# Kernel optimization log

Hardware: AMD Instinct MI355X
Metric: run time of the kernel (lower is better)

Reference implementation:

```python
import jax, jax.numpy as jnp
import numpy as np

I16_MIN, I16_MAX = -32768, 32767
NUM_SEG = 8


def setup_inputs() -> dict:
    key = jax.random.key(0)
    k1, k2, k3, k4, k5, k6 = jax.random.split(key, 6)
    # Float activation; quantized to qint16 inside the op via input_scale.
    x = jax.random.normal(k1, (16, 1024, 2048), dtype=jnp.float32)
    input_scale = jnp.full((1,), 1.0 / 8192.0, dtype=jnp.float32)  # randn*8192 spans most of int16
    out_scale = jnp.full((1,), 1e-3, dtype=jnp.float32)
    # Per-segment fixed-point linear coefficients (as produced by _convert_linear_kb / toqint):
    # 16-bit k, wide b pre-shifted by left_shift, result right-shifted by right_shift.
    alpha = jax.random.randint(k2, (NUM_SEG,), -4096, 4096, dtype=jnp.int32)        # int16 k
    beta = jax.random.randint(k3, (NUM_SEG,), -(1 << 20), 1 << 20, dtype=jnp.int32)  # int b
    left_shift = jax.random.randint(k4, (NUM_SEG,), 0, 5, dtype=jnp.int32)           # int8 shift
    right_shift = jax.random.randint(k5, (NUM_SEG,), 1, 15, dtype=jnp.int32)         # int8 shift
    # Sorted segment upper bounds in quantized domain; last entry pinned to qint16 max
    # (mirrors `segment_max[-1] = info.max` in _init_multi_table_params).
    segment_max = jnp.sort(jax.random.randint(k6, (NUM_SEG,), I16_MIN, I16_MAX, dtype=jnp.int32))
    segment_max = segment_max.at[-1].set(I16_MAX)
    return dict(x=x, input_scale=input_scale, out_scale=out_scale, alpha=alpha,
                beta=beta, left_shift=left_shift, right_shift=right_shift,
                segment_max=segment_max)


def reference(x, input_scale, out_scale, alpha, beta, left_shift, right_shift, segment_max):
    # Quantize input to qint16 (scale-only, zero_point = 0 as in the module).
    xi = jnp.clip(jnp.round(x / input_scale), I16_MIN, I16_MAX).astype(jnp.int32)
    # Segment selection: element belongs to the first segment whose upper bound >= xi.
    idx = jnp.clip(jnp.searchsorted(segment_max, xi, side='left'), 0, NUM_SEG - 1)
    # Gather per-segment fixed-point coefficients.
    k = alpha[idx]
    b = beta[idx]
    ls = left_shift[idx]
    rs = right_shift[idx]
    # Hardware shift-multiply-add: acc = k*x + (b << left_shift), then rounded
    # arithmetic right shift by right_shift, saturate to qint16.
    acc = k * xi + jnp.left_shift(b, ls)
    round_bias = jnp.where(rs > 0, jnp.left_shift(jnp.int32(1), jnp.maximum(rs - 1, 0)), jnp.int32(0))
    qy = jnp.clip(jnp.right_shift(acc + round_bias, rs), I16_MIN, I16_MAX)
    # Dequantized output (QTensor data * out_scale, zero_point = 0).
    return qy.astype(jnp.float32) * out_scale
```

## Files before the change

kernel.cpp:

```cpp
#include <hip/hip_runtime.h>


typedef float f32x4 __attribute__((ext_vector_type(4)));

__device__ __forceinline__ float seg_one(float x, float inv_s,
                                         float sm0, float sm1, float sm2, float sm3,
                                         float sm4, float sm5, float sm6,
                                         const float2* tab, float olo, float ohi)
{
    float xf = rintf(x * inv_s);
    xf = __builtin_amdgcn_fmed3f(xf, -32768.0f, 32767.0f);
    int idx = (sm0 < xf) + (sm1 < xf) + (sm2 < xf) + (sm3 < xf)
            + (sm4 < xf) + (sm5 < xf) + (sm6 < xf);
    float2 t = tab[idx];
    float y = fmaf(t.x, xf, t.y);
    return __builtin_amdgcn_fmed3f(y, olo, ohi);
}

__global__ __launch_bounds__(256) void SegmentLUT_83021717831949_kernel(
    const float* __restrict__ x,
    const float* __restrict__ input_scale,
    const float* __restrict__ out_scale,
    const int*   __restrict__ alpha,
    const int*   __restrict__ beta,
    const int*   __restrict__ lsh,
    const int*   __restrict__ rsh,
    const int*   __restrict__ smax,
    float*       __restrict__ out,
    int n)
{
    __shared__ float2 tab[8];
    float os = out_scale[0];
    if (threadIdx.x < 8) {
        int j  = (int)threadIdx.x;
        int rs = rsh[j];
        int rm1 = rs - 1 > 0 ? rs - 1 : 0;
        int rbias = rs > 0 ? (1 << rm1) : 0;
        int bc = (int)((unsigned)beta[j] << (lsh[j] & 31)) + rbias;
        float sc = ldexpf(os, -rs);
        tab[j] = make_float2((float)alpha[j] * sc, (float)bc * sc);
    }
    float inv_s = 1.0f / input_scale[0];
    float sm0 = (float)smax[0], sm1 = (float)smax[1], sm2 = (float)smax[2];
    float sm3 = (float)smax[3], sm4 = (float)smax[4], sm5 = (float)smax[5];
    float sm6 = (float)smax[6];
    float olo = -32768.0f * os, ohi = 32767.0f * os;
    __syncthreads();

    int nvec   = n >> 2;
    int stride = (int)(gridDim.x * blockDim.x);
    int tid    = (int)(blockIdx.x * blockDim.x + threadIdx.x);

    const f32x4* __restrict__ xv = (const f32x4*)x;
    f32x4* __restrict__ ov = (f32x4*)out;

#define SEG1(e) seg_one((e), inv_s, sm0, sm1, sm2, sm3, sm4, sm5, sm6, tab, olo, ohi)
#define SEG4(o, v) do { \
        (o).x = SEG1((v).x); (o).y = SEG1((v).y); \
        (o).z = SEG1((v).z); (o).w = SEG1((v).w); } while (0)

    int i = tid;
    for (; i + 3 * stride < nvec; i += 4 * stride) {
        f32x4 v0 = xv[i];
        f32x4 v1 = xv[i + stride];
        f32x4 v2 = xv[i + 2 * stride];
        f32x4 v3 = xv[i + 3 * stride];
        f32x4 o0, o1, o2, o3;
        SEG4(o0, v0);
        SEG4(o1, v1);
        SEG4(o2, v2);
        SEG4(o3, v3);
        __builtin_nontemporal_store(o0, &ov[i]);
        __builtin_nontemporal_store(o1, &ov[i + stride]);
        __builtin_nontemporal_store(o2, &ov[i + 2 * stride]);
        __builtin_nontemporal_store(o3, &ov[i + 3 * stride]);
    }
    for (; i < nvec; i += stride) {
        f32x4 v = xv[i];
        f32x4 o;
        SEG4(o, v);
        __builtin_nontemporal_store(o, &ov[i]);
    }
    for (int k = (nvec << 2) + tid; k < n; k += stride) {
        out[k] = SEG1(x[k]);
    }
#undef SEG4
#undef SEG1
}

extern "C" void kernel_launch(void* const* d_in, const int* in_sizes, int n_in,
                              void* d_out, int out_size, void* d_ws, size_t ws_size,
                              hipStream_t stream) {
    const float* x           = (const float*)d_in[0];
    const float* input_scale = (const float*)d_in[1];
    const float* out_scale   = (const float*)d_in[2];
    const int*   alpha       = (const int*)d_in[3];
    const int*   beta        = (const int*)d_in[4];
    const int*   lsh         = (const int*)d_in[5];
    const int*   rsh         = (const int*)d_in[6];
    const int*   smax        = (const int*)d_in[7];
    float* out = (float*)d_out;

    int n = in_sizes[0];
    int nvec = n >> 2;
    int blocks = (nvec + 255) / 256;
    if (blocks > 2048) blocks = 2048;
    if (blocks < 1) blocks = 1;

    SegmentLUT_83021717831949_kernel<<<blocks, 256, 0, stream>>>(
        x, input_scale, out_scale, alpha, beta, lsh, rsh, smax, out, n);
}
```

Before: 251.1 us.

## Replace grid-stride loop with one-vector-per-thread launch and early load

Drops the capped grid-stride loop and instead launches one thread per float4 across the whole tensor. Each thread issues its global load before the per-block table setup and barrier, so the load latency overlaps that setup. Stores become ordinary rather than nontemporal. The cost is many more blocks (about 32K), each redoing the table setup, the scalar parameter loads and a barrier.

```diff
diff --git a/kernel.cpp b/kernel.cpp
--- a/kernel.cpp
+++ b/kernel.cpp
@@ -29,6 +29,14 @@
     float*       __restrict__ out,
     int n)
 {
+    int nvec = n >> 2;
+    int i = (int)(blockIdx.x * blockDim.x + threadIdx.x);
+    bool valid = i < nvec;
+
+    const f32x4* __restrict__ xv = (const f32x4*)x;
+    f32x4 v = {};
+    if (valid) v = xv[i];
+
     __shared__ float2 tab[8];
     float os = out_scale[0];
     if (threadIdx.x < 8) {
@@ -47,45 +55,19 @@
     float olo = -32768.0f * os, ohi = 32767.0f * os;
     __syncthreads();
 
-    int nvec   = n >> 2;
-    int stride = (int)(gridDim.x * blockDim.x);
-    int tid    = (int)(blockIdx.x * blockDim.x + threadIdx.x);
-
-    const f32x4* __restrict__ xv = (const f32x4*)x;
-    f32x4* __restrict__ ov = (f32x4*)out;
-
-#define SEG1(e) seg_one((e), inv_s, sm0, sm1, sm2, sm3, sm4, sm5, sm6, tab, olo, ohi)
-#define SEG4(o, v) do { \
-        (o).x = SEG1((v).x); (o).y = SEG1((v).y); \
-        (o).z = SEG1((v).z); (o).w = SEG1((v).w); } while (0)
-
-    int i = tid;
-    for (; i + 3 * stride < nvec; i += 4 * stride) {
-        f32x4 v0 = xv[i];
-        f32x4 v1 = xv[i + stride];
-        f32x4 v2 = xv[i + 2 * stride];
-        f32x4 v3 = xv[i + 3 * stride];
-        f32x4 o0, o1, o2, o3;
-        SEG4(o0, v0);
-        SEG4(o1, v1);
-        SEG4(o2, v2);
-        SEG4(o3, v3);
-        __builtin_nontemporal_store(o0, &ov[i]);
-        __builtin_nontemporal_store(o1, &ov[i + stride]);
-        __builtin_nontemporal_store(o2, &ov[i + 2 * stride]);
-        __builtin_nontemporal_store(o3, &ov[i + 3 * stride]);
+    if (valid) {
+        f32x4 o;
+        o.x = seg_one(v.x, inv_s, sm0, sm1, sm2, sm3, sm4, sm5, sm6, tab, olo, ohi);
+        o.y = seg_one(v.y, inv_s, sm0, sm1, sm2, sm3, sm4, sm5, sm6, tab, olo, ohi);
+        o.z = seg_one(v.z, inv_s, sm0, sm1, sm2, sm3, sm4, sm5, sm6, tab, olo, ohi);
+        o.w = seg_one(v.w, inv_s, sm0, sm1, sm2, sm3, sm4, sm5, sm6, tab, olo, ohi);
+        ((f32x4*)out)[i] = o;
     }
-    for (; i < nvec; i += stride) {
-        f32x4 v = xv[i];
-        f32x4 o;
-        SEG4(o, v);
-        __builtin_nontemporal_store(o, &ov[i]);
+    int ntail = n & 3;
+    if (ntail && i < ntail) {
+        int k = (nvec << 2) + i;
+        out[k] = seg_one(x[k], inv_s, sm0, sm1, sm2, sm3, sm4, sm5, sm6, tab, olo, ohi);
     }
-    for (int k = (nvec << 2) + tid; k < n; k += stride) {
-        out[k] = SEG1(x[k]);
-    }
-#undef SEG4
-#undef SEG1
 }
 
 extern "C" void kernel_launch(void* const* d_in, const int* in_sizes, int n_in,
@@ -104,7 +86,6 @@
     int n = in_sizes[0];
     int nvec = n >> 2;
     int blocks = (nvec + 255) / 256;
-    if (blocks > 2048) blocks = 2048;
     if (blocks < 1) blocks = 1;
 
     SegmentLUT_83021717831949_kernel<<<blocks, 256, 0, stream>>>(
```

New measurement: 228.6 us. -9.0%, faster.

## Replace grid-stride loop with one-shot grid issuing loads before table setup

Applied to the files above, without the earlier changes.

The persistent grid-stride loop capped at 2048 blocks is replaced by a grid sized so each thread handles exactly four float4 vectors. The input loads are issued at kernel entry, before the shared LUT setup and barrier, so memory latency overlaps the table construction. Output stores become ordinary stores instead of nontemporal ones. This launches many more short-lived blocks, so the per-block setup (coefficient table, scalar loads) runs far more often. Losing the nontemporal hint may also change cache behaviour for the streaming writes.

```diff
diff --git a/kernel.cpp b/kernel.cpp
--- a/kernel.cpp
+++ b/kernel.cpp
@@ -29,6 +29,18 @@
     float*       __restrict__ out,
     int n)
 {
+    int nvec   = n >> 2;
+    int stride = (int)(gridDim.x * blockDim.x);
+    int i0 = (int)(blockIdx.x * blockDim.x + threadIdx.x);
+    int i1 = i0 + stride, i2 = i0 + 2 * stride, i3 = i0 + 3 * stride;
+
+    const f32x4* __restrict__ xv = (const f32x4*)x;
+    f32x4 v0 = {}, v1 = {}, v2 = {}, v3 = {};
+    if (i0 < nvec) v0 = xv[i0];
+    if (i1 < nvec) v1 = xv[i1];
+    if (i2 < nvec) v2 = xv[i2];
+    if (i3 < nvec) v3 = xv[i3];
+
     __shared__ float2 tab[8];
     float os = out_scale[0];
     if (threadIdx.x < 8) {
@@ -47,41 +59,26 @@
     float olo = -32768.0f * os, ohi = 32767.0f * os;
     __syncthreads();
 
-    int nvec   = n >> 2;
-    int stride = (int)(gridDim.x * blockDim.x);
-    int tid    = (int)(blockIdx.x * blockDim.x + threadIdx.x);
-
-    const f32x4* __restrict__ xv = (const f32x4*)x;
-    f32x4* __restrict__ ov = (f32x4*)out;
-
 #define SEG1(e) seg_one((e), inv_s, sm0, sm1, sm2, sm3, sm4, sm5, sm6, tab, olo, ohi)
 #define SEG4(o, v) do { \
         (o).x = SEG1((v).x); (o).y = SEG1((v).y); \
         (o).z = SEG1((v).z); (o).w = SEG1((v).w); } while (0)
 
-    int i = tid;
-    for (; i + 3 * stride < nvec; i += 4 * stride) {
-        f32x4 v0 = xv[i];
-        f32x4 v1 = xv[i + stride];
-        f32x4 v2 = xv[i + 2 * stride];
-        f32x4 v3 = xv[i + 3 * stride];
-        f32x4 o0, o1, o2, o3;
-        SEG4(o0, v0);
-        SEG4(o1, v1);
-        SEG4(o2, v2);
-        SEG4(o3, v3);
-        __builtin_nontemporal_store(o0, &ov[i]);
-        __builtin_nontemporal_store(o1, &ov[i + stride]);
-        __builtin_nontemporal_store(o2, &ov[i + 2 * stride]);
-        __builtin_nontemporal_store(o3, &ov[i + 3 * stride]);
-    }
-    for (; i < nvec; i += stride) {
-        f32x4 v = xv[i];
-        f32x4 o;
-        SEG4(o, v);
-        __builtin_nontemporal_store(o, &ov[i]);
-    }
-    for (int k = (nvec << 2) + tid; k < n; k += stride) {
+    f32x4 o0, o1, o2, o3;
+    SEG4(o0, v0);
+    SEG4(o1, v1);
+    SEG4(o2, v2);
+    SEG4(o3, v3);
+
+    f32x4* __restrict__ ov = (f32x4*)out;
+    if (i0 < nvec) ov[i0] = o0;
+    if (i1 < nvec) ov[i1] = o1;
+    if (i2 < nvec) ov[i2] = o2;
+    if (i3 < nvec) ov[i3] = o3;
+
+    int ntail = n & 3;
+    if (ntail && i0 < ntail) {
+        int k = (nvec << 2) + i0;
         out[k] = SEG1(x[k]);
     }
 #undef SEG4
@@ -103,8 +100,8 @@
 
     int n = in_sizes[0];
     int nvec = n >> 2;
-    int blocks = (nvec + 255) / 256;
-    if (blocks > 2048) blocks = 2048;
+    int threads_needed = (nvec + 3) / 4;
+    int blocks = (threads_needed + 255) / 256;
     if (blocks < 1) blocks = 1;
 
     SegmentLUT_83021717831949_kernel<<<blocks, 256, 0, stream>>>(
```

After: 247.4 us. No clear change (-1.5%).
